# Kernel optimization log

Measured on AMD Instinct MI355X. Metric: run time of the kernel, lower is better.

## Reference

```python
import jax, jax.numpy as jnp
import numpy as np
from jax import lax

NUM_HEADS = 8
DIM = 384
B, H, W = 4, 128, 128
NEG_INF = -1e30


def setup_inputs() -> dict:
    key = jax.random.key(0)
    ks = jax.random.split(key, 5)
    x = jax.random.normal(ks[0], (B, DIM, H, W), dtype=jnp.float32)
    qkv_w = jax.random.normal(ks[1], (3 * DIM, DIM), dtype=jnp.float32) * 0.02   # 1x1 conv weight
    dw_w = jax.random.normal(ks[2], (3 * DIM, 1, 3, 3), dtype=jnp.float32) * 0.02  # depthwise 3x3
    proj_w = jax.random.normal(ks[3], (DIM, DIM), dtype=jnp.float32) * 0.02     # 1x1 conv weight
    temperature = jnp.ones((NUM_HEADS, 1, 1), dtype=jnp.float32)
    a1 = jnp.array([0.2], dtype=jnp.float32)
    a2 = jnp.array([0.2], dtype=jnp.float32)
    a3 = jnp.array([0.2], dtype=jnp.float32)
    a4 = jnp.array([0.2], dtype=jnp.float32)
    return {"x": x, "qkv_w": qkv_w, "dw_w": dw_w, "proj_w": proj_w,
            "temperature": temperature, "a1": a1, "a2": a2, "a3": a3, "a4": a4}


def _topk_softmax(attn, k):
    # keep top-k along last dim, softmax over kept entries (threshold == k-th largest)
    thr = lax.top_k(attn, k)[0][..., -1:]
    return jax.nn.softmax(jnp.where(attn >= thr, attn, NEG_INF), axis=-1)


def reference(x, qkv_w, dw_w, proj_w, temperature, a1, a2, a3, a4):
    b, c, h, w = x.shape
    head = NUM_HEADS
    C = c // head          # per-head channel dim (48)
    n = h * w              # token dim

    qkv = jnp.einsum('bchw,oc->bohw', x, qkv_w)  # 1x1 conv, no bias
    qkv = lax.conv_general_dilated(
        qkv, dw_w, window_strides=(1, 1), padding='SAME',
        feature_group_count=3 * c,
        dimension_numbers=('NCHW', 'OIHW', 'NCHW'))  # depthwise 3x3
    q, k, v = jnp.split(qkv, 3, axis=1)

    def heads(t):
        return t.reshape(b, head, C, n)  # b head c (h w)
    q, k, v = heads(q), heads(k), heads(v)

    q = q / jnp.linalg.norm(q, axis=-1, keepdims=True)
    k = k / jnp.linalg.norm(k, axis=-1, keepdims=True)

    attn = jnp.einsum('bhcn,bhdn->bhcd', q, k) * temperature  # [b,head,C,C]

    ks = [int(C / 2), int(C * 2 / 3), int(C * 3 / 4), int(C * 4 / 5)]
    weights = [a1, a2, a3, a4]
    out = jnp.zeros_like(v)
    for kk, a in zip(ks, weights):
        p = _topk_softmax(attn, kk)
        out = out + a * jnp.einsum('bhcd,bhdn->bhcn', p, v)

    out = out.reshape(b, c, h, w)
    out = jnp.einsum('bchw,oc->bohw', out, proj_w)  # 1x1 conv project_out
    return out
```

## Files before the change

### kernel.cpp

```cpp
#include <hip/hip_runtime.h>

#define NHEADS 8
#define DIM 384
#define BB 4
#define HW 16384
#define CPH 48

typedef unsigned int u32;
typedef _Float16 f16x8 __attribute__((ext_vector_type(8)));
typedef _Float16 f16x4 __attribute__((ext_vector_type(4)));
typedef __attribute__((ext_vector_type(4))) float f32x4;

__device__ __forceinline__ float wave_min(float v) {
    #pragma unroll
    for (int off = 32; off; off >>= 1) v = fminf(v, __shfl_xor(v, off));
    return v;
}
__device__ __forceinline__ float wave_max(float v) {
    #pragma unroll
    for (int off = 32; off; off >>= 1) v = fmaxf(v, __shfl_xor(v, off));
    return v;
}
__device__ __forceinline__ float wave_sum(float v) {
    #pragma unroll
    for (int off = 32; off; off >>= 1) v += __shfl_xor(v, off);
    return v;
}

#define GLOBAL_TO_LDS16(gsrc, ldst)                                           \
    __builtin_amdgcn_global_load_lds(                                         \
        (const __attribute__((address_space(1))) u32*)(gsrc),                 \
        (__attribute__((address_space(3))) u32*)(ldst), 16, 0, 0)

__global__ void cvt_w(const float* __restrict__ a, _Float16* __restrict__ o, int n)
{
    const int i = blockIdx.x * 256 + threadIdx.x;
    if (i < n) o[i] = (_Float16)a[i];
}

__global__ __launch_bounds__(256) void transpose_cvt(
    const float* __restrict__ x, _Float16* __restrict__ xt)
{
    const int n  = blockIdx.x * 256 + threadIdx.x;
    const int c0 = blockIdx.y * 16;
    const int b  = blockIdx.z;
    const float* xp = x + ((size_t)b * DIM + c0) * HW + n;
    alignas(16) _Float16 th[16];
    #pragma unroll
    for (int j = 0; j < 16; ++j) th[j] = (_Float16)xp[(size_t)j * HW];
    _Float16* op = xt + ((size_t)b * HW + n) * DIM + c0;
    *(f16x8*)&op[0] = *(const f16x8*)&th[0];
    *(f16x8*)&op[8] = *(const f16x8*)&th[8];
}

__global__ __launch_bounds__(256) void gemm_f16(
    const _Float16* __restrict__ W, const _Float16* __restrict__ Xt,
    void* __restrict__ Y, int out_f32)
{
    const int n0 = blockIdx.x * 128;
    const int m0 = blockIdx.y * 128;
    const int b  = blockIdx.z;

    __shared__ _Float16 sA[128 * 32];
    __shared__ _Float16 sB[128 * 32];

    const int t = threadIdx.x;
    const int w = t >> 6;
    const int l = t & 63;

    const _Float16* gA = W  + ((size_t)(m0 + w * 32 + (l >> 2))) * DIM + (l & 3) * 8;
    const _Float16* gB = Xt + ((size_t)b * HW + n0 + w * 32 + (l >> 2)) * DIM + (l & 3) * 8;
    _Float16* lA = &sA[(w * 32) * 32];
    _Float16* lB = &sB[(w * 32) * 32];

    f32x4 acc[4][4];
    #pragma unroll
    for (int i = 0; i < 4; ++i)
        #pragma unroll
        for (int j = 0; j < 4; ++j)
            acc[i][j] = (f32x4){0.f, 0.f, 0.f, 0.f};

    const int wm = (w >> 1) * 64, wn = (w & 1) * 64;
    const int fr = l & 15, fk = (l >> 4) * 8;

    for (int k0 = 0; k0 < DIM; k0 += 32) {
        __syncthreads();
        GLOBAL_TO_LDS16(gA + k0,             lA);
        GLOBAL_TO_LDS16(gA + k0 + 16 * DIM,  lA + 16 * 32);
        GLOBAL_TO_LDS16(gB + k0,             lB);
        GLOBAL_TO_LDS16(gB + k0 + 16 * DIM,  lB + 16 * 32);
        __syncthreads();

        f16x8 af[4], bfv[4];
        #pragma unroll
        for (int mi = 0; mi < 4; ++mi)
            af[mi] = *(const f16x8*)&sA[(wm + mi * 16 + fr) * 32 + fk];
        #pragma unroll
        for (int ni = 0; ni < 4; ++ni)
            bfv[ni] = *(const f16x8*)&sB[(wn + ni * 16 + fr) * 32 + fk];
        #pragma unroll
        for (int mi = 0; mi < 4; ++mi)
            #pragma unroll
            for (int ni = 0; ni < 4; ++ni)
                acc[mi][ni] = __builtin_amdgcn_mfma_f32_16x16x32_f16(
                    af[mi], bfv[ni], acc[mi][ni], 0, 0, 0);
    }

    const int er = (l >> 4) * 4;
    if (out_f32) {
        float* Yp = (float*)Y + (size_t)b * DIM * HW;
        #pragma unroll
        for (int mi = 0; mi < 4; ++mi)
            #pragma unroll
            for (int ni = 0; ni < 4; ++ni)
                #pragma unroll
                for (int r = 0; r < 4; ++r)
                    Yp[(size_t)(m0 + wm + mi * 16 + er + r) * HW + n0 + wn + ni * 16 + fr]
                        = acc[mi][ni][r];
    } else {
        _Float16* Yp = (_Float16*)Y + (size_t)b * DIM * HW;
        #pragma unroll
        for (int mi = 0; mi < 4; ++mi)
            #pragma unroll
            for (int ni = 0; ni < 4; ++ni)
                #pragma unroll
                for (int r = 0; r < 4; ++r)
                    Yp[(size_t)(m0 + wm + mi * 16 + er + r) * HW + n0 + wn + ni * 16 + fr]
                        = (_Float16)acc[mi][ni][r];
    }
}

__global__ __launch_bounds__(256) void dwconv_f16(
    const _Float16* __restrict__ in, const float* __restrict__ w9,
    _Float16* __restrict__ out, float* __restrict__ ss, int ss_off)
{
    const int j  = blockIdx.x & 3;
    const int p  = blockIdx.x >> 2;
    const int cl = p % DIM;
    const int b  = p / DIM;
    const int r0 = j * 32;

    __shared__ __align__(16) _Float16 tile[34 * 136 + 8];
    const int t = threadIdx.x;

    const uint4 z4 = make_uint4(0, 0, 0, 0);
    for (int i = t; i < 579; i += 256)
        *(uint4*)&tile[i * 8] = z4;
    __syncthreads();

    const _Float16* ip = in + (size_t)p * HW;
    for (int c = t; c < 34 * 16; c += 256) {
        const int i = c >> 4, seg = c & 15;
        const int g = r0 - 1 + i;
        if ((unsigned)g < 128u)
            *(f16x8*)&tile[i * 136 + 8 + seg * 8] = *(const f16x8*)&ip[g * 128 + seg * 8];
    }

    float w[9];
    #pragma unroll
    for (int i = 0; i < 9; ++i) w[i] = w9[cl * 9 + i];
    __syncthreads();

    const int yr = t >> 3;
    const int xc = (t & 7) * 16;

    float acc[16];
    #pragma unroll
    for (int c = 0; c < 16; ++c) acc[c] = 0.f;

    #pragma unroll
    for (int dy = 0; dy < 3; ++dy) {
        const _Float16* rp = &tile[(yr + dy) * 136 + xc];
        const f16x8 v0 = *(const f16x8*)&rp[0];
        const f16x8 v1 = *(const f16x8*)&rp[8];
        const f16x8 v2 = *(const f16x8*)&rp[16];
        const f16x8 v3 = *(const f16x8*)&rp[24];
        float rv[18];
        #pragma unroll
        for (int i = 0; i < 18; ++i) {
            const int idx = 7 + i;
            const _Float16 h = (idx < 8)  ? v0[idx]
                             : (idx < 16) ? v1[idx - 8]
                             : (idx < 24) ? v2[idx - 16]
                                          : v3[idx - 24];
            rv[i] = (float)h;
        }
        const float w0 = w[dy * 3 + 0], w1 = w[dy * 3 + 1], w2 = w[dy * 3 + 2];
        #pragma unroll
        for (int c = 0; c < 16; ++c) {
            acc[c] = fmaf(rv[c],     w0, acc[c]);
            acc[c] = fmaf(rv[c + 1], w1, acc[c]);
            acc[c] = fmaf(rv[c + 2], w2, acc[c]);
        }
    }

    alignas(16) _Float16 oh[16];
    float ssum = 0.f;
    #pragma unroll
    for (int c = 0; c < 16; ++c) {
        oh[c] = (_Float16)acc[c];
        ssum = fmaf(acc[c], acc[c], ssum);
    }
    _Float16* op = out + (size_t)p * HW + (r0 + yr) * 128 + xc;
    *(f16x8*)&op[0] = *(const f16x8*)&oh[0];
    *(f16x8*)&op[8] = *(const f16x8*)&oh[8];

    if (ss != nullptr) {
        __syncthreads();
        float* red = (float*)tile;
        red[t] = ssum;
        __syncthreads();
        for (int s = 128; s > 0; s >>= 1) {
            if (t < s) red[t] += red[t + s];
            __syncthreads();
        }
        if (t == 0) atomicAdd(&ss[b * (2 * DIM) + ss_off + cl], red[0]);
    }
}

#define GNC 1024
__global__ __launch_bounds__(256) void gram_qk(
    const _Float16* __restrict__ qA, const _Float16* __restrict__ kA,
    float* __restrict__ G)
{
    const int n0 = blockIdx.x * GNC;
    const int h  = blockIdx.y;
    const int b  = blockIdx.z;
    const _Float16* qb = qA + ((size_t)b * DIM + h * CPH) * HW + n0;
    const _Float16* kb = kA + ((size_t)b * DIM + h * CPH) * HW + n0;

    const int t = threadIdx.x;
    const int w = t >> 6, l = t & 63;
    const int fr = l & 15, fk = (l >> 4) * 8;

    f32x4 acc[3][3];
    #pragma unroll
    for (int i = 0; i < 3; ++i)
        #pragma unroll
        for (int j = 0; j < 3; ++j)
            acc[i][j] = (f32x4){0.f, 0.f, 0.f, 0.f};

    const int nbase = w * (GNC / 4);
    #pragma unroll 4
    for (int nn = 0; nn < GNC / 4; nn += 32) {
        f16x8 qf[3], kf[3];
        #pragma unroll
        for (int i = 0; i < 3; ++i) {
            const size_t off = (size_t)(i * 16 + fr) * HW + nbase + nn + fk;
            qf[i] = *(const f16x8*)&qb[off];
            kf[i] = *(const f16x8*)&kb[off];
        }
        #pragma unroll
        for (int i = 0; i < 3; ++i)
            #pragma unroll
            for (int j = 0; j < 3; ++j)
                acc[i][j] = __builtin_amdgcn_mfma_f32_16x16x32_f16(
                    qf[i], kf[j], acc[i][j], 0, 0, 0);
    }

    __shared__ float red[4][CPH * CPH];
    const int er = (l >> 4) * 4;
    #pragma unroll
    for (int i = 0; i < 3; ++i)
        #pragma unroll
        for (int j = 0; j < 3; ++j)
            #pragma unroll
            for (int r = 0; r < 4; ++r)
                red[w][(i * 16 + er + r) * CPH + j * 16 + fr] = acc[i][j][r];
    __syncthreads();

    float* Gp = G + ((size_t)(b * NHEADS + h)) * CPH * CPH;
    for (int i = t; i < CPH * CPH; i += 256)
        atomicAdd(&Gp[i], red[0][i] + red[1][i] + red[2][i] + red[3][i]);
}

__global__ __launch_bounds__(64) void topk_combine(
    const float* __restrict__ G, const float* __restrict__ ss,
    const float* __restrict__ temp,
    const float* __restrict__ a1, const float* __restrict__ a2,
    const float* __restrict__ a3, const float* __restrict__ a4,
    float* __restrict__ P)
{
    const int row = blockIdx.x;
    const int bh  = row / CPH;
    const int r   = row - bh * CPH;
    const int b = bh >> 3, h = bh & 7;
    const int l = threadIdx.x;

    const float tpr = temp[h];
    const float* ssb = ss + b * (2 * DIM);
    const float invq = 1.f / sqrtf(ssb[h * CPH + r]);

    float att = -3.0e38f;
    if (l < CPH)
        att = G[(size_t)row * CPH + l] * invq * (1.f / sqrtf(ssb[DIM + h * CPH + l])) * tpr;

    int cnt = 0;
    #pragma unroll
    for (int i = 0; i < CPH; ++i)
        cnt += (__shfl(att, i) > att) ? 1 : 0;

    const float mx   = wave_max(att);
    const float thr0 = wave_min((l < CPH && cnt < 24) ? att : 3.0e38f);
    const float thr1 = wave_min((l < CPH && cnt < 32) ? att : 3.0e38f);
    const float thr2 = wave_min((l < CPH && cnt < 36) ? att : 3.0e38f);
    const float thr3 = wave_min((l < CPH && cnt < 38) ? att : 3.0e38f);

    const float e = (l < CPH) ? expf(att - mx) : 0.f;
    const float Z0 = wave_sum(att >= thr0 ? e : 0.f);
    const float Z1 = wave_sum(att >= thr1 ? e : 0.f);
    const float Z2 = wave_sum(att >= thr2 ? e : 0.f);
    const float Z3 = wave_sum(att >= thr3 ? e : 0.f);

    const float w0 = a1[0] / Z0, w1 = a2[0] / Z1, w2 = a3[0] / Z2, w3 = a4[0] / Z3;
    float pv = 0.f;
    if (att >= thr0) pv += w0 * e;
    if (att >= thr1) pv += w1 * e;
    if (att >= thr2) pv += w2 * e;
    if (att >= thr3) pv += w3 * e;
    if (l < CPH) P[(size_t)row * CPH + l] = pv;
}

__global__ __launch_bounds__(256) void pv_apply(
    const _Float16* __restrict__ v, const float* __restrict__ P,
    _Float16* __restrict__ out1t)
{
    const int bh = blockIdx.y;
    const int b = bh >> 3, h = bh & 7;
    const int n0 = blockIdx.x * 256;

    __shared__ float sPT[CPH][52];
    __shared__ __align__(16) _Float16 sO[256 * 48];
    const int t = threadIdx.x;
    for (int i = t; i < CPH * CPH; i += 256) {
        const int c = i / CPH, d = i % CPH;
        sPT[d][c] = P[(size_t)bh * CPH * CPH + i];
    }
    __syncthreads();

    const int cg = t >> 6;
    const int lane = t & 63;
    const _Float16* vb = v + ((size_t)b * DIM + h * CPH) * HW + n0 + lane * 4;

    float acc[12][4];
    #pragma unroll
    for (int i = 0; i < 12; ++i)
        #pragma unroll
        for (int jn = 0; jn < 4; ++jn) acc[i][jn] = 0.f;

    for (int d = 0; d < CPH; ++d) {
        const f16x4 vv = *(const f16x4*)&vb[(size_t)d * HW];
        const float vvs[4] = {(float)vv[0], (float)vv[1], (float)vv[2], (float)vv[3]};
        #pragma unroll
        for (int cq = 0; cq < 3; ++cq) {
            const float4 pc = *(const float4*)&sPT[d][cg * 12 + cq * 4];
            const float pcs[4] = {pc.x, pc.y, pc.z, pc.w};
            #pragma unroll
            for (int a = 0; a < 4; ++a)
                #pragma unroll
                for (int jn = 0; jn < 4; ++jn)
                    acc[cq * 4 + a][jn] = fmaf(pcs[a], vvs[jn], acc[cq * 4 + a][jn]);
        }
    }

    #pragma unroll
    for (int jn = 0; jn < 4; ++jn)
        #pragma unroll
        for (int cq = 0; cq < 3; ++cq)
            #pragma unroll
            for (int a = 0; a < 4; ++a)
                sO[(lane * 4 + jn) * 48 + cg * 12 + cq * 4 + a]
                    = (_Float16)acc[cq * 4 + a][jn];
    __syncthreads();

    _Float16* dst = out1t + ((size_t)b * HW + n0 + t) * DIM + h * CPH;
    #pragma unroll
    for (int i = 0; i < 6; ++i)
        *(f16x8*)&dst[i * 8] = *(const f16x8*)&sO[t * 48 + i * 8];
}

extern "C" void kernel_launch(void* const* d_in, const int* in_sizes, int n_in,
                              void* d_out, int out_size, void* d_ws, size_t ws_size,
                              hipStream_t stream)
{
    const float* x      = (const float*)d_in[0];
    const float* qkv_w  = (const float*)d_in[1];
    const float* dw_w   = (const float*)d_in[2];
    const float* proj_w = (const float*)d_in[3];
    const float* temp   = (const float*)d_in[4];
    const float* a1 = (const float*)d_in[5];
    const float* a2 = (const float*)d_in[6];
    const float* a3 = (const float*)d_in[7];
    const float* a4 = (const float*)d_in[8];
    float* out = (float*)d_out;

    const size_t PBE = (size_t)HW * DIM;
    const size_t WQE = (size_t)1152 * 384;
    const size_t WPE = (size_t)384 * 384;

    auto need_for = [&](size_t nb) -> size_t {
        return nb * PBE * 2 * 4 + (WQE + WPE) * 2
             + (nb * 768 + 2 * nb * NHEADS * CPH * CPH) * 4;
    };

    int nb, npass;
    if      (ws_size >= need_for(4)) { nb = 4; npass = 1; }
    else if (ws_size >= need_for(2)) { nb = 2; npass = 2; }
    else if (ws_size >= need_for(1)) { nb = 1; npass = 4; }
    else return;

    _Float16* A  = (_Float16*)d_ws;
    _Float16* C  = A + (size_t)nb * PBE;
    _Float16* D  = C + (size_t)nb * PBE;
    _Float16* E  = D + (size_t)nb * PBE;
    _Float16* wq = E + (size_t)nb * PBE;
    _Float16* wp = wq + WQE;
    float* buf_ss = (float*)(wp + WPE);
    float* buf_G  = buf_ss + (size_t)nb * 768;
    float* buf_P  = buf_G + (size_t)nb * NHEADS * CPH * CPH;

    cvt_w<<<dim3((1152 * 384 + 255) / 256), 256, 0, stream>>>(qkv_w, wq, 1152 * 384);
    cvt_w<<<dim3((384 * 384 + 255) / 256), 256, 0, stream>>>(proj_w, wp, 384 * 384);

    for (int p = 0; p < npass; ++p) {
        const int b0 = p * nb;
        const float* xp   = x   + (size_t)b0 * PBE;
        float*       outp = out + (size_t)b0 * PBE;

        const dim3 ggrid(HW / 128, DIM / 128, nb);
        const dim3 dgrid(nb * DIM * 4);

        transpose_cvt<<<dim3(HW / 256, DIM / 16, nb), 256, 0, stream>>>(xp, A);
        hipMemsetAsync(buf_ss, 0,
                       ((size_t)nb * 768 + (size_t)nb * NHEADS * CPH * CPH) * sizeof(float),
                       stream);

        gemm_f16<<<ggrid, 256, 0, stream>>>(wq, A, C, 0);
        dwconv_f16<<<dgrid, 256, 0, stream>>>(C, dw_w, D, buf_ss, 0);
        gemm_f16<<<ggrid, 256, 0, stream>>>(wq + (size_t)DIM * DIM, A, C, 0);
        dwconv_f16<<<dgrid, 256, 0, stream>>>(C, dw_w + (size_t)DIM * 9, E, buf_ss, DIM);

        gram_qk<<<dim3(HW / GNC, NHEADS, nb), 256, 0, stream>>>(D, E, buf_G);
        topk_combine<<<dim3(nb * NHEADS * CPH), 64, 0, stream>>>(
            buf_G, buf_ss, temp, a1, a2, a3, a4, buf_P);

        gemm_f16<<<ggrid, 256, 0, stream>>>(wq + (size_t)2 * DIM * DIM, A, C, 0);
        dwconv_f16<<<dgrid, 256, 0, stream>>>(C, dw_w + (size_t)2 * DIM * 9, D, nullptr, 0);

        pv_apply<<<dim3(HW / 256, nb * NHEADS), 256, 0, stream>>>(D, buf_P, A);

        gemm_f16<<<ggrid, 256, 0, stream>>>(wp, A, outp, 1);
    }
}
```

Measured before the change: 497.4 us.

## Fold attention P matrix into projection weights, replacing pv_apply with transpose

Rather than applying the per-head 48x48 P matrix to V and then running the projection GEMM, this precomputes a per-batch fused weight Wf = proj_w · blockdiag(P) and runs the final GEMM on transposed V directly. pv_apply is replaced by a small fuse_pw kernel plus a plain fp16 transpose, and the transpose kernels now handle 32 channels per thread instead of 16. This removes the FMA-heavy pv pass but adds per-batch weights, extra workspace, and a second rounding of the combined weight to fp16.

```diff
diff --git a/kernel.cpp b/kernel.cpp
--- a/kernel.cpp
+++ b/kernel.cpp
@@ -42,20 +42,37 @@
     const float* __restrict__ x, _Float16* __restrict__ xt)
 {
     const int n  = blockIdx.x * 256 + threadIdx.x;
-    const int c0 = blockIdx.y * 16;
+    const int c0 = blockIdx.y * 32;
     const int b  = blockIdx.z;
     const float* xp = x + ((size_t)b * DIM + c0) * HW + n;
-    alignas(16) _Float16 th[16];
-    #pragma unroll
-    for (int j = 0; j < 16; ++j) th[j] = (_Float16)xp[(size_t)j * HW];
+    alignas(16) _Float16 th[32];
+    #pragma unroll
+    for (int j = 0; j < 32; ++j) th[j] = (_Float16)xp[(size_t)j * HW];
     _Float16* op = xt + ((size_t)b * HW + n) * DIM + c0;
-    *(f16x8*)&op[0] = *(const f16x8*)&th[0];
-    *(f16x8*)&op[8] = *(const f16x8*)&th[8];
+    #pragma unroll
+    for (int i = 0; i < 4; ++i)
+        *(f16x8*)&op[i * 8] = *(const f16x8*)&th[i * 8];
+}
+
+__global__ __launch_bounds__(256) void transpose16(
+    const _Float16* __restrict__ in, _Float16* __restrict__ ot)
+{
+    const int n  = blockIdx.x * 256 + threadIdx.x;
+    const int c0 = blockIdx.y * 32;
+    const int b  = blockIdx.z;
+    const _Float16* ip = in + ((size_t)b * DIM + c0) * HW + n;
+    alignas(16) _Float16 th[32];
+    #pragma unroll
+    for (int j = 0; j < 32; ++j) th[j] = ip[(size_t)j * HW];
+    _Float16* op = ot + ((size_t)b * HW + n) * DIM + c0;
+    #pragma unroll
+    for (int i = 0; i < 4; ++i)
+        *(f16x8*)&op[i * 8] = *(const f16x8*)&th[i * 8];
 }
 
 __global__ __launch_bounds__(256) void gemm_f16(
     const _Float16* __restrict__ W, const _Float16* __restrict__ Xt,
-    void* __restrict__ Y, int out_f32)
+    void* __restrict__ Y, int out_f32, int wbs)
 {
     const int n0 = blockIdx.x * 128;
     const int m0 = blockIdx.y * 128;
@@ -68,7 +85,8 @@
     const int w = t >> 6;
     const int l = t & 63;
 
-    const _Float16* gA = W  + ((size_t)(m0 + w * 32 + (l >> 2))) * DIM + (l & 3) * 8;
+    const _Float16* gA = W + (size_t)b * wbs
+                           + ((size_t)(m0 + w * 32 + (l >> 2))) * DIM + (l & 3) * 8;
     const _Float16* gB = Xt + ((size_t)b * HW + n0 + w * 32 + (l >> 2)) * DIM + (l & 3) * 8;
     _Float16* lA = &sA[(w * 32) * 32];
     _Float16* lB = &sB[(w * 32) * 32];
@@ -321,62 +339,29 @@
     if (l < CPH) P[(size_t)row * CPH + l] = pv;
 }
 
-__global__ __launch_bounds__(256) void pv_apply(
-    const _Float16* __restrict__ v, const float* __restrict__ P,
-    _Float16* __restrict__ out1t)
-{
-    const int bh = blockIdx.y;
-    const int b = bh >> 3, h = bh & 7;
-    const int n0 = blockIdx.x * 256;
-
-    __shared__ float sPT[CPH][52];
-    __shared__ __align__(16) _Float16 sO[256 * 48];
+__global__ __launch_bounds__(256) void fuse_pw(
+    const float* __restrict__ pw, const float* __restrict__ P,
+    _Float16* __restrict__ Wf)
+{
+    const int h = blockIdx.x;
+    const int b = blockIdx.y;
     const int t = threadIdx.x;
-    for (int i = t; i < CPH * CPH; i += 256) {
-        const int c = i / CPH, d = i % CPH;
-        sPT[d][c] = P[(size_t)bh * CPH * CPH + i];
-    }
+
+    __shared__ float sP[CPH][CPH];
+    for (int i = t; i < CPH * CPH; i += 256)
+        sP[i / CPH][i % CPH] = P[((size_t)(b * NHEADS + h)) * CPH * CPH + i];
     __syncthreads();
 
-    const int cg = t >> 6;
-    const int lane = t & 63;
-    const _Float16* vb = v + ((size_t)b * DIM + h * CPH) * HW + n0 + lane * 4;
-
-    float acc[12][4];
-    #pragma unroll
-    for (int i = 0; i < 12; ++i)
-        #pragma unroll
-        for (int jn = 0; jn < 4; ++jn) acc[i][jn] = 0.f;
-
-    for (int d = 0; d < CPH; ++d) {
-        const f16x4 vv = *(const f16x4*)&vb[(size_t)d * HW];
-        const float vvs[4] = {(float)vv[0], (float)vv[1], (float)vv[2], (float)vv[3]};
-        #pragma unroll
-        for (int cq = 0; cq < 3; ++cq) {
-            const float4 pc = *(const float4*)&sPT[d][cg * 12 + cq * 4];
-            const float pcs[4] = {pc.x, pc.y, pc.z, pc.w};
-            #pragma unroll
-            for (int a = 0; a < 4; ++a)
-                #pragma unroll
-                for (int jn = 0; jn < 4; ++jn)
-                    acc[cq * 4 + a][jn] = fmaf(pcs[a], vvs[jn], acc[cq * 4 + a][jn]);
-        }
-    }
-
-    #pragma unroll
-    for (int jn = 0; jn < 4; ++jn)
-        #pragma unroll
-        for (int cq = 0; cq < 3; ++cq)
-            #pragma unroll
-            for (int a = 0; a < 4; ++a)
-                sO[(lane * 4 + jn) * 48 + cg * 12 + cq * 4 + a]
-                    = (_Float16)acc[cq * 4 + a][jn];
-    __syncthreads();
-
-    _Float16* dst = out1t + ((size_t)b * HW + n0 + t) * DIM + h * CPH;
-    #pragma unroll
-    for (int i = 0; i < 6; ++i)
-        *(f16x8*)&dst[i * 8] = *(const f16x8*)&sO[t * 48 + i * 8];
+    for (int idx = t; idx < DIM * CPH; idx += 256) {
+        const int o = idx / CPH;
+        const int d = idx - o * CPH;
+        const float* pwr = pw + (size_t)o * DIM + h * CPH;
+        float s = 0.f;
+        #pragma unroll
+        for (int c = 0; c < CPH; ++c)
+            s = fmaf(pwr[c], sP[c][d], s);
+        Wf[((size_t)b * DIM + o) * DIM + h * CPH + d] = (_Float16)s;
+    }
 }
 
 extern "C" void kernel_launch(void* const* d_in, const int* in_sizes, int n_in,
@@ -399,7 +384,7 @@
     const size_t WPE = (size_t)384 * 384;
 
     auto need_for = [&](size_t nb) -> size_t {
-        return nb * PBE * 2 * 4 + (WQE + WPE) * 2
+        return nb * PBE * 2 * 4 + (WQE + nb * WPE) * 2
              + (nb * 768 + 2 * nb * NHEADS * CPH * CPH) * 4;
     };
 
@@ -414,13 +399,12 @@
     _Float16* D  = C + (size_t)nb * PBE;
     _Float16* E  = D + (size_t)nb * PBE;
     _Float16* wq = E + (size_t)nb * PBE;
-    _Float16* wp = wq + WQE;
-    float* buf_ss = (float*)(wp + WPE);
+    _Float16* Wf = wq + WQE;
+    float* buf_ss = (float*)(Wf + (size_t)nb * WPE);
     float* buf_G  = buf_ss + (size_t)nb * 768;
     float* buf_P  = buf_G + (size_t)nb * NHEADS * CPH * CPH;
 
     cvt_w<<<dim3((1152 * 384 + 255) / 256), 256, 0, stream>>>(qkv_w, wq, 1152 * 384);
-    cvt_w<<<dim3((384 * 384 + 255) / 256), 256, 0, stream>>>(proj_w, wp, 384 * 384);
 
     for (int p = 0; p < npass; ++p) {
         const int b0 = p * nb;
@@ -429,26 +413,29 @@
 
         const dim3 ggrid(HW / 128, DIM / 128, nb);
         const dim3 dgrid(nb * DIM * 4);
-
-        transpose_cvt<<<dim3(HW / 256, DIM / 16, nb), 256, 0, stream>>>(xp, A);
+        const dim3 tgrid(HW / 256, DIM / 32, nb);
+
+        transpose_cvt<<<tgrid, 256, 0, stream>>>(xp, A);
         hipMemsetAsync(buf_ss, 0,
                        ((size_t)nb * 768 + (size_t)nb * NHEADS * CPH * CPH) * sizeof(float),
                        stream);
 
-        gemm_f16<<<ggrid, 256, 0, stream>>>(wq, A, C, 0);
+        gemm_f16<<<ggrid, 256, 0, stream>>>(wq, A, C, 0, 0);
         dwconv_f16<<<dgrid, 256, 0, stream>>>(C, dw_w, D, buf_ss, 0);
-        gemm_f16<<<ggrid, 256, 0, stream>>>(wq + (size_t)DIM * DIM, A, C, 0);
+        gemm_f16<<<ggrid, 256, 0, stream>>>(wq + (size_t)DIM * DIM, A, C, 0, 0);
         dwconv_f16<<<dgrid, 256, 0, stream>>>(C, dw_w + (size_t)DIM * 9, E, buf_ss, DIM);
 
         gram_qk<<<dim3(HW / GNC, NHEADS, nb), 256, 0, stream>>>(D, E, buf_G);
         topk_combine<<<dim3(nb * NHEADS * CPH), 64, 0, stream>>>(
             buf_G, buf_ss, temp, a1, a2, a3, a4, buf_P);
 
-        gemm_f16<<<ggrid, 256, 0, stream>>>(wq + (size_t)2 * DIM * DIM, A, C, 0);
+        gemm_f16<<<ggrid, 256, 0, stream>>>(wq + (size_t)2 * DIM * DIM, A, C, 0, 0);
         dwconv_f16<<<dgrid, 256, 0, stream>>>(C, dw_w + (size_t)2 * DIM * 9, D, nullptr, 0);
 
-        pv_apply<<<dim3(HW / 256, nb * NHEADS), 256, 0, stream>>>(D, buf_P, A);
-
-        gemm_f16<<<ggrid, 256, 0, stream>>>(wp, A, outp, 1);
-    }
-}
+        fuse_pw<<<dim3(NHEADS, nb), 256, 0, stream>>>(proj_w, buf_P, Wf);
+
+        transpose16<<<tgrid, 256, 0, stream>>>(D, A);
+
+        gemm_f16<<<ggrid, 256, 0, stream>>>(Wf, A, outp, 1, (int)WPE);
+    }
+}
```

New measurement: 544.2 us. 9.4% more time.
